# Kernel tuning notes

Hardware: AMD Instinct MI355X
Metric: run time of the kernel (lower is better)

## Reference

```python
import jax, jax.numpy as jnp
import numpy as np

CONF_THRESH = 0.01
TOP_K = 200
NMS_THRESH = 0.45


def decode(loc, dbox):
    # loc, dbox: [N,4]; dbox is (cx, cy, w, h)
    cxcy = dbox[:, :2] + loc[:, :2] * 0.1 * dbox[:, 2:]
    wh = dbox[:, 2:] * jnp.exp(loc[:, 2:] * 0.2)
    xymin = cxcy - wh * 0.5
    xymax = xymin + wh
    return jnp.concatenate([xymin, xymax], axis=1)  # [N,4] (x1,y1,x2,y2)


def nms_class(scores, boxes):
    # scores: [N], boxes: [N,4]. Mirrors torch greedy NMS with fixed-size padding.
    masked = jnp.where(scores > CONF_THRESH, scores, -1.0)
    topv, topi = jax.lax.top_k(masked, TOP_K)  # descending score, like idx[-top_k:] reversed
    cb = boxes[topi]  # [K,4]
    valid = topv > CONF_THRESH
    x1, y1, x2, y2 = cb[:, 0], cb[:, 1], cb[:, 2], cb[:, 3]
    area = (x2 - x1) * (y2 - y1)
    ar = jnp.arange(TOP_K)

    def body(i, keep):
        cur = keep[i]
        w = jnp.clip(jnp.minimum(x2, x2[i]) - jnp.maximum(x1, x1[i]), 0.0)
        h = jnp.clip(jnp.minimum(y2, y2[i]) - jnp.maximum(y1, y1[i]), 0.0)
        inter = w * h
        iou = inter / (area - inter + area[i])  # union = rem_area - inter + area[i]
        sup = (iou > NMS_THRESH) & (ar > i) & cur
        return keep & (~sup)

    keep = jax.lax.fori_loop(0, TOP_K, body, valid)
    # compact kept rows to the front, preserving descending-score order (stable sort)
    order = jnp.argsort(jnp.logical_not(keep), stable=True)
    count = jnp.sum(keep)
    rows = jnp.concatenate([topv[:, None], cb], axis=1)[order]  # [K,5] = (score, x1,y1,x2,y2)
    return jnp.where(ar[:, None] < count, rows, 0.0)


def setup_inputs() -> dict:
    key = jax.random.key(0)
    k1, k2, k3, k4 = jax.random.split(key, 4)
    B, N, C = 128, 8732, 21
    loc_data = jax.random.normal(k1, (B, N, 4), dtype=jnp.float32) * 0.5
    conf_data = jax.random.normal(k2, (B, N, C), dtype=jnp.float32)
    centers = jax.random.uniform(k3, (N, 2), dtype=jnp.float32)
    wh = jax.random.uniform(k4, (N, 2), dtype=jnp.float32, minval=0.02, maxval=0.3)
    dbox_list = jnp.concatenate([centers, wh], axis=1)
    return {"loc_data": loc_data, "conf_data": conf_data, "dbox_list": dbox_list}


def reference(loc_data, conf_data, dbox_list):
    conf = jax.nn.softmax(conf_data, axis=-1)                              # [B,N,C]
    boxes = jax.vmap(decode, in_axes=(0, None))(loc_data, dbox_list)       # [B,N,4]
    # vmap over classes (axis 1 of per-image conf) then over batch
    per_cls = jax.vmap(jax.vmap(nms_class, in_axes=(1, None)),
                       in_axes=(0, 0))(conf, boxes)                        # [B,C,K,5]
    return per_cls.at[:, 0].set(0.0)  # class 0 (background) is skipped in torch
```

## Files before the change

kernel.cpp:

```cpp
#include <hip/hip_runtime.h>

#define N_ANCH 8732
#define NCLS   21
#define BATCH  128
#define TOPK   200
#define CONF_T 0.01f
#define NMS_T  0.45f
#define HSIZE  1024
#define CAND_MAX 1024
#define NQ4    2183

__device__ __forceinline__ float exp_np(float x) {
    const float fx = floorf(__fmaf_rn(x, 1.442695040888963f, 0.5f));
    float t = __fmaf_rn(fx, -0.693359375f, x);
    t = __fmaf_rn(fx, 2.12194440e-4f, t);
    const float z = __fmul_rn(t, t);
    float y = 1.9875691500e-4f;
    y = __fmaf_rn(y, t, 1.3981999507e-3f);
    y = __fmaf_rn(y, t, 8.3334519073e-3f);
    y = __fmaf_rn(y, t, 4.1665795894e-2f);
    y = __fmaf_rn(y, t, 1.6666665459e-1f);
    y = __fmaf_rn(y, t, 5.0000001201e-1f);
    y = __fmaf_rn(y, z, t);
    y = __fadd_rn(y, 1.0f);
    return ldexpf(y, (int)fx);
}

__global__ __launch_bounds__(256) void prep_kernel(
    const float* __restrict__ loc, const float* __restrict__ conf,
    const float* __restrict__ dbox, float* __restrict__ probs,
    float* __restrict__ boxes)
{
    __shared__ float srow[256 * NCLS];
    const int block_row0 = blockIdx.x * 256;
    const float* cbase = conf + (size_t)block_row0 * NCLS;
    for (int i = threadIdx.x; i < 256 * NCLS; i += 256) srow[i] = cbase[i];
    __syncthreads();

    const int row = block_row0 + threadIdx.x;
    const int b = row / N_ANCH;
    const int n = row - b * N_ANCH;

    float e[NCLS];
    float m = srow[threadIdx.x * NCLS];
#pragma unroll
    for (int c = 1; c < NCLS; ++c) m = fmaxf(m, srow[threadIdx.x * NCLS + c]);
#pragma unroll
    for (int c = 0; c < NCLS; ++c)
        e[c] = exp_np(__fsub_rn(srow[threadIdx.x * NCLS + c], m));

    float acc[16];
#pragma unroll
    for (int j = 0; j < 16; ++j) acc[j] = e[j];
#pragma unroll
    for (int j = 0; j < 5; ++j) acc[j] = __fadd_rn(acc[j], e[16 + j]);
    float u[8];
#pragma unroll
    for (int j = 0; j < 8; ++j) u[j] = __fadd_rn(acc[j], acc[j + 8]);
    const float v0 = __fadd_rn(u[0], u[4]), v1 = __fadd_rn(u[1], u[5]);
    const float v2 = __fadd_rn(u[2], u[6]), v3 = __fadd_rn(u[3], u[7]);
    const float w0 = __fadd_rn(v0, v2), w1 = __fadd_rn(v1, v3);
    const float s  = __fadd_rn(w0, w1);

#pragma unroll
    for (int c = 1; c < NCLS; ++c)
        probs[((size_t)b * 20 + (c - 1)) * N_ANCH + n] = __fdiv_rn(e[c], s);

    const float4 l = *(const float4*)(loc + (size_t)row * 4);
    const float4 d = *(const float4*)(dbox + (size_t)n * 4);
    const float cx = __fmaf_rn(__fmul_rn(l.x, 0.1f), d.z, d.x);
    const float cy = __fmaf_rn(__fmul_rn(l.y, 0.1f), d.w, d.y);
    const float w  = __fmul_rn(d.z, exp_np(__fmul_rn(l.z, 0.2f)));
    const float h  = __fmul_rn(d.w, exp_np(__fmul_rn(l.w, 0.2f)));
    const float x1 = __fmaf_rn(w, -0.5f, cx);
    const float y1 = __fmaf_rn(h, -0.5f, cy);
    float4 o; o.x = x1; o.y = y1; o.z = __fadd_rn(x1, w); o.w = __fadd_rn(y1, h);
    *(float4*)(boxes + (size_t)row * 4) = o;
}

__global__ __launch_bounds__(256) void sel_kernel(
    const float* __restrict__ probs, const float* __restrict__ boxes,
    float* __restrict__ probs_mut)
{
    const int task = blockIdx.x;
    const int b = task / NCLS;
    const int c = task - b * NCLS;
    const int tid = threadIdx.x;
    if (c == 0) return;

    const float* prow = probs + ((size_t)b * 20 + (c - 1)) * N_ANCH;

    __shared__ int hist2[HSIZE * 2];
    __shared__ int wsum[4];
    __shared__ unsigned long long cand[CAND_MAX];
    __shared__ int selB;
    __shared__ int cnts[2];
    __shared__ unsigned ck[TOPK];
    __shared__ int  cn[TOPK];
    __shared__ unsigned sk[TOPK];
    __shared__ int  sn_[TOPK];

    const int wid = tid >> 6, lane = tid & 63;
    const int par = wid & 1;

    for (int i = tid; i < HSIZE * 2; i += 256) hist2[i] = 0;
    __syncthreads();
    for (int idx = tid; idx < NQ4; idx += 256) {
        const float4 v = *(const float4*)(prow + idx * 4);
        if (v.x > CONF_T) atomicAdd(&hist2[(int)((__float_as_uint(v.x) >> 16) - 0x3C23u) * 2 + par], 1);
        if (v.y > CONF_T) atomicAdd(&hist2[(int)((__float_as_uint(v.y) >> 16) - 0x3C23u) * 2 + par], 1);
        if (v.z > CONF_T) atomicAdd(&hist2[(int)((__float_as_uint(v.z) >> 16) - 0x3C23u) * 2 + par], 1);
        if (v.w > CONF_T) atomicAdd(&hist2[(int)((__float_as_uint(v.w) >> 16) - 0x3C23u) * 2 + par], 1);
    }
    __syncthreads();

    const int hbase = HSIZE - 4 * (tid + 1);
    int hb[4];
#pragma unroll
    for (int j = 0; j < 4; ++j) hb[j] = hist2[(hbase + j) * 2] + hist2[(hbase + j) * 2 + 1];
    const int part = hb[0] + hb[1] + hb[2] + hb[3];

    int incl = part;
#pragma unroll
    for (int off = 1; off < 64; off <<= 1) {
        const int v = __shfl_up(incl, off);
        if (lane >= off) incl += v;
    }
    if (lane == 63) wsum[wid] = incl;
    __syncthreads();
    int pre = 0;
    for (int w = 0; w < wid; ++w) pre += wsum[w];
    const int excl  = pre + incl - part;
    const int total = wsum[0] + wsum[1] + wsum[2] + wsum[3];
    if (tid == 0 && total < TOPK) selB = -1;
    if (excl < TOPK && excl + part >= TOPK) {
        int cacc = excl;
        for (int j = 3; j >= 0; --j) {
            if (cacc + hb[j] >= TOPK) { selB = hbase + j; break; }
            cacc += hb[j];
        }
    }
    if (tid == 0) { cnts[0] = 0; cnts[1] = 0; }
    __syncthreads();
    const int B = selB;

    for (int idx = tid; idx < NQ4; idx += 256) {
        const float4 v = *(const float4*)(prow + idx * 4);
        const float vv[4] = {v.x, v.y, v.z, v.w};
#pragma unroll
        for (int q = 0; q < 4; ++q) {
            const float s = vv[q];
            if (s > CONF_T) {
                const unsigned kk = __float_as_uint(s);
                const int bkt = (int)((kk >> 16) - 0x3C23u);
                if (bkt > B) {
                    const int p = atomicAdd(&cnts[0], 1);
                    ck[p] = kk; cn[p] = idx * 4 + q;
                } else if (bkt == B) {
                    const int qq = atomicAdd(&cnts[1], 1);
                    if (qq < CAND_MAX)
                        cand[qq] = ((unsigned long long)kk << 32) | (unsigned)(~(idx * 4 + q));
                }
            }
        }
    }
    __syncthreads();
    const int ndef  = cnts[0];
    const int slots = TOPK - ndef;
    int cc = cnts[1]; if (cc > CAND_MAX) cc = CAND_MAX;
    for (int i = tid; i < cc; i += 256) {
        const unsigned long long mine = cand[i];
        int rank = 0;
        for (int j = 0; j < cc; ++j) rank += (cand[j] > mine) ? 1 : 0;
        if (rank < slots) {
            const int p = atomicAdd(&cnts[0], 1);
            ck[p] = (unsigned)(mine >> 32);
            cn[p] = (int)(~(unsigned)mine);
        }
    }
    __syncthreads();
    const int cnt_arr = cnts[0];

    if (tid < TOPK) { sk[tid] = 0u; sn_[tid] = -1; }
    __syncthreads();
    if (tid < cnt_arr) {
        const unsigned mk = ck[tid];
        const int mn = cn[tid];
        int rank = 0;
        for (int j = 0; j < cnt_arr; ++j) {
            const unsigned kj = ck[j];
            rank += (kj > mk || (kj == mk && cn[j] < mn)) ? 1 : 0;
        }
        sk[rank] = mk; sn_[rank] = mn;
    }
    __syncthreads();

    float* selrow = probs_mut + ((size_t)b * 20 + (c - 1)) * N_ANCH;
    for (int i = tid; i < TOPK; i += 256) {
        const int n = sn_[i];
        float scv = 0.f;
        float4 bx = make_float4(0.f, 0.f, 0.f, 0.f);
        if (n >= 0) {
            scv = __uint_as_float(sk[i]);
            bx = *(const float4*)(boxes + ((size_t)b * N_ANCH + n) * 4);
        }
        float* dst = selrow + i * 5;
        dst[0] = scv; dst[1] = bx.x; dst[2] = bx.y; dst[3] = bx.z; dst[4] = bx.w;
    }
}

__global__ __launch_bounds__(256) void nms_kernel(
    const float* __restrict__ sel, float* __restrict__ out)
{
    const int wv = threadIdx.x >> 6;
    const int lane = threadIdx.x & 63;
    const int task = blockIdx.x * 4 + wv;
    const int b = task / NCLS;
    const int c = task - b * NCLS;
    float* obase = out + (size_t)task * (TOPK * 5);
    __shared__ float outrow[4][TOPK * 5];

    if (c == 0) {
        for (int i = lane; i < TOPK * 5; i += 64) obase[i] = 0.f;
        return;
    }
    const float* srow = sel + ((size_t)b * 20 + (c - 1)) * N_ANCH;

    float sc[4], x1[4], y1[4], x2[4], y2[4], ar[4];
    int kp[4];
#pragma unroll
    for (int s = 0; s < 4; ++s) {
        const int i = s * 64 + lane;
        float a = 0.f, p1 = 0.f, p2 = 0.f, p3 = 0.f, p4 = 0.f;
        if (i < TOPK) {
            a  = srow[i * 5 + 0];
            p1 = srow[i * 5 + 1]; p2 = srow[i * 5 + 2];
            p3 = srow[i * 5 + 3]; p4 = srow[i * 5 + 4];
        }
        sc[s] = a; x1[s] = p1; y1[s] = p2; x2[s] = p3; y2[s] = p4;
        ar[s] = __fmul_rn(__fsub_rn(p3, p1), __fsub_rn(p4, p2));
        kp[s] = (a > CONF_T) ? 1 : 0;
    }

#pragma unroll
    for (int si = 0; si < 4; ++si) {
        const int ilim = (si < 3) ? 64 : (TOPK - 192);
        for (int o = 0; o < ilim; ++o) {
            const int ki = __shfl(kp[si], o);
            if (!ki) continue;
            const float ix1 = __shfl(x1[si], o);
            const float iy1 = __shfl(y1[si], o);
            const float ix2 = __shfl(x2[si], o);
            const float iy2 = __shfl(y2[si], o);
            const float ia  = __shfl(ar[si], o);
            if (lane > o && (si * 64 + lane) < TOPK && kp[si]) {
                const float w = fmaxf(0.f, __fsub_rn(fminf(x2[si], ix2), fmaxf(x1[si], ix1)));
                const float h = fmaxf(0.f, __fsub_rn(fminf(y2[si], iy2), fmaxf(y1[si], iy1)));
                const float inter = __fmul_rn(w, h);
                const float denom = __fadd_rn(__fsub_rn(ar[si], inter), ia);
                if (__fdiv_rn(inter, denom) > NMS_T) kp[si] = 0;
            }
#pragma unroll
            for (int s = si + 1; s < 4; ++s) {
                const int j = s * 64 + lane;
                if (j < TOPK && kp[s]) {
                    const float w = fmaxf(0.f, __fsub_rn(fminf(x2[s], ix2), fmaxf(x1[s], ix1)));
                    const float h = fmaxf(0.f, __fsub_rn(fminf(y2[s], iy2), fmaxf(y1[s], iy1)));
                    const float inter = __fmul_rn(w, h);
                    const float denom = __fadd_rn(__fsub_rn(ar[s], inter), ia);
                    if (__fdiv_rn(inter, denom) > NMS_T) kp[s] = 0;
                }
            }
        }
    }

    unsigned long long msk[4];
#pragma unroll
    for (int s = 0; s < 4; ++s) msk[s] = __ballot(kp[s] != 0);
    const unsigned long long lt = (1ull << lane) - 1ull;

    for (int i = lane; i < TOPK * 5; i += 64) outrow[wv][i] = 0.f;
    int base = 0;
#pragma unroll
    for (int s = 0; s < 4; ++s) {
        if (kp[s]) {
            const int d = base + (int)__popcll(msk[s] & lt);
            outrow[wv][d * 5 + 0] = sc[s];
            outrow[wv][d * 5 + 1] = x1[s];
            outrow[wv][d * 5 + 2] = y1[s];
            outrow[wv][d * 5 + 3] = x2[s];
            outrow[wv][d * 5 + 4] = y2[s];
        }
        base += (int)__popcll(msk[s]);
    }
    for (int i = lane; i < TOPK * 5; i += 64) obase[i] = outrow[wv][i];
}

extern "C" void kernel_launch(void* const* d_in, const int* in_sizes, int n_in,
                              void* d_out, int out_size, void* d_ws, size_t ws_size,
                              hipStream_t stream) {
    (void)in_sizes; (void)n_in; (void)out_size; (void)ws_size;
    const float* loc  = (const float*)d_in[0];
    const float* conf = (const float*)d_in[1];
    const float* dbox = (const float*)d_in[2];
    float* out   = (float*)d_out;
    float* probs = (float*)d_ws;
    float* boxes = (float*)((char*)d_ws + (size_t)BATCH * 20 * N_ANCH * 4);

    prep_kernel<<<(BATCH * N_ANCH) / 256, 256, 0, stream>>>(loc, conf, dbox, probs, boxes);
    sel_kernel<<<BATCH * NCLS, 256, 0, stream>>>(probs, boxes, probs);
    nms_kernel<<<(BATCH * NCLS) / 4, 256, 0, stream>>>(probs, out);
}
```

Before: 198.3 us.

## Restructure NMS into parallel IoU bitmask build plus serial mask sweep

Each (batch,class) task now gets a full 256-thread block instead of one wavefront. The four waves compute a full pairwise IoU suppression bitmask matrix in parallel into shared memory. A cheap serial sweep over 64-bit masks then resolves greedy keep, and compaction uses popcount/bit selection. This removes the serialized shuffle-and-divide chain per kept box. The cost is computing all pairwise IoUs regardless of early suppression, a redundant per-thread sweep, and four times more blocks.

Result: slower. 277.7 us (+40.1%).

```diff
diff --git a/kernel.cpp b/kernel.cpp
--- a/kernel.cpp
+++ b/kernel.cpp
@@ -212,88 +212,113 @@
 __global__ __launch_bounds__(256) void nms_kernel(
     const float* __restrict__ sel, float* __restrict__ out)
 {
-    const int wv = threadIdx.x >> 6;
-    const int lane = threadIdx.x & 63;
-    const int task = blockIdx.x * 4 + wv;
+    const int task = blockIdx.x;
     const int b = task / NCLS;
     const int c = task - b * NCLS;
     float* obase = out + (size_t)task * (TOPK * 5);
-    __shared__ float outrow[4][TOPK * 5];
+    const int tid = threadIdx.x;
+    const int wv = tid >> 6, lane = tid & 63;
 
     if (c == 0) {
-        for (int i = lane; i < TOPK * 5; i += 64) obase[i] = 0.f;
+        for (int i = tid; i < TOPK * 5; i += 256) obase[i] = 0.f;
         return;
     }
     const float* srow = sel + ((size_t)b * 20 + (c - 1)) * N_ANCH;
 
-    float sc[4], x1[4], y1[4], x2[4], y2[4], ar[4];
-    int kp[4];
+    __shared__ float bxs[TOPK * 5];
+    __shared__ unsigned long long rows[TOPK][4];
+    __shared__ unsigned long long Ksh[4];
+
+    for (int i = tid; i < TOPK * 5; i += 256) bxs[i] = srow[i];
+    __syncthreads();
+
+    float jx1[4], jy1[4], jx2[4], jy2[4], jar[4];
+    int jval[4];
 #pragma unroll
     for (int s = 0; s < 4; ++s) {
-        const int i = s * 64 + lane;
+        const int j = s * 64 + lane;
         float a = 0.f, p1 = 0.f, p2 = 0.f, p3 = 0.f, p4 = 0.f;
-        if (i < TOPK) {
-            a  = srow[i * 5 + 0];
-            p1 = srow[i * 5 + 1]; p2 = srow[i * 5 + 2];
-            p3 = srow[i * 5 + 3]; p4 = srow[i * 5 + 4];
-        }
-        sc[s] = a; x1[s] = p1; y1[s] = p2; x2[s] = p3; y2[s] = p4;
-        ar[s] = __fmul_rn(__fsub_rn(p3, p1), __fsub_rn(p4, p2));
-        kp[s] = (a > CONF_T) ? 1 : 0;
-    }
-
-#pragma unroll
-    for (int si = 0; si < 4; ++si) {
-        const int ilim = (si < 3) ? 64 : (TOPK - 192);
-        for (int o = 0; o < ilim; ++o) {
-            const int ki = __shfl(kp[si], o);
-            if (!ki) continue;
-            const float ix1 = __shfl(x1[si], o);
-            const float iy1 = __shfl(y1[si], o);
-            const float ix2 = __shfl(x2[si], o);
-            const float iy2 = __shfl(y2[si], o);
-            const float ia  = __shfl(ar[si], o);
-            if (lane > o && (si * 64 + lane) < TOPK && kp[si]) {
-                const float w = fmaxf(0.f, __fsub_rn(fminf(x2[si], ix2), fmaxf(x1[si], ix1)));
-                const float h = fmaxf(0.f, __fsub_rn(fminf(y2[si], iy2), fmaxf(y1[si], iy1)));
-                const float inter = __fmul_rn(w, h);
-                const float denom = __fadd_rn(__fsub_rn(ar[si], inter), ia);
-                if (__fdiv_rn(inter, denom) > NMS_T) kp[si] = 0;
-            }
-#pragma unroll
-            for (int s = si + 1; s < 4; ++s) {
-                const int j = s * 64 + lane;
-                if (j < TOPK && kp[s]) {
-                    const float w = fmaxf(0.f, __fsub_rn(fminf(x2[s], ix2), fmaxf(x1[s], ix1)));
-                    const float h = fmaxf(0.f, __fsub_rn(fminf(y2[s], iy2), fmaxf(y1[s], iy1)));
-                    const float inter = __fmul_rn(w, h);
-                    const float denom = __fadd_rn(__fsub_rn(ar[s], inter), ia);
-                    if (__fdiv_rn(inter, denom) > NMS_T) kp[s] = 0;
-                }
-            }
-        }
-    }
-
-    unsigned long long msk[4];
-#pragma unroll
-    for (int s = 0; s < 4; ++s) msk[s] = __ballot(kp[s] != 0);
-    const unsigned long long lt = (1ull << lane) - 1ull;
-
-    for (int i = lane; i < TOPK * 5; i += 64) outrow[wv][i] = 0.f;
-    int base = 0;
-#pragma unroll
-    for (int s = 0; s < 4; ++s) {
-        if (kp[s]) {
-            const int d = base + (int)__popcll(msk[s] & lt);
-            outrow[wv][d * 5 + 0] = sc[s];
-            outrow[wv][d * 5 + 1] = x1[s];
-            outrow[wv][d * 5 + 2] = y1[s];
-            outrow[wv][d * 5 + 3] = x2[s];
-            outrow[wv][d * 5 + 4] = y2[s];
-        }
-        base += (int)__popcll(msk[s]);
-    }
-    for (int i = lane; i < TOPK * 5; i += 64) obase[i] = outrow[wv][i];
+        if (j < TOPK) {
+            a = bxs[j * 5 + 0];
+            p1 = bxs[j * 5 + 1]; p2 = bxs[j * 5 + 2];
+            p3 = bxs[j * 5 + 3]; p4 = bxs[j * 5 + 4];
+        }
+        jx1[s] = p1; jy1[s] = p2; jx2[s] = p3; jy2[s] = p4;
+        jar[s] = __fmul_rn(__fsub_rn(p3, p1), __fsub_rn(p4, p2));
+        jval[s] = (a > CONF_T) ? 1 : 0;
+    }
+    if (wv == 0) {
+#pragma unroll
+        for (int s = 0; s < 4; ++s) {
+            const unsigned long long m = __ballot(jval[s] != 0);
+            if (lane == 0) Ksh[s] = m;
+        }
+    }
+
+    const int i0 = wv * 50;
+    for (int i = i0; i < i0 + 50; ++i) {
+        const float ix1 = bxs[i * 5 + 1], iy1 = bxs[i * 5 + 2];
+        const float ix2 = bxs[i * 5 + 3], iy2 = bxs[i * 5 + 4];
+        const float ia  = __fmul_rn(__fsub_rn(ix2, ix1), __fsub_rn(iy2, iy1));
+#pragma unroll
+        for (int s = 0; s < 4; ++s) {
+            const int j = s * 64 + lane;
+            const float w = fmaxf(0.f, __fsub_rn(fminf(jx2[s], ix2), fmaxf(jx1[s], ix1)));
+            const float h = fmaxf(0.f, __fsub_rn(fminf(jy2[s], iy2), fmaxf(jy1[s], iy1)));
+            const float inter = __fmul_rn(w, h);
+            const float denom = __fadd_rn(__fsub_rn(jar[s], inter), ia);
+            const float iou = __fdiv_rn(inter, denom);
+            const bool bit = (j < TOPK) && (j > i) && (iou > NMS_T);
+            const unsigned long long m = __ballot(bit);
+            if (lane == 0) rows[i][s] = m;
+        }
+    }
+    __syncthreads();
+
+    unsigned long long K0 = Ksh[0], K1 = Ksh[1], K2 = Ksh[2], K3 = Ksh[3];
+#pragma unroll
+    for (int w4 = 0; w4 < 4; ++w4) {
+        const int lim = (w4 < 3) ? 64 : (TOPK - 192);
+        for (int o = 0; o < lim; ++o) {
+            const int i = w4 * 64 + o;
+            unsigned long long live;
+            if (w4 == 0) live = (K0 >> o) & 1ull;
+            else if (w4 == 1) live = (K1 >> o) & 1ull;
+            else if (w4 == 2) live = (K2 >> o) & 1ull;
+            else live = (K3 >> o) & 1ull;
+            const unsigned long long msel = 0ull - live;
+            K0 &= ~(rows[i][0] & msel);
+            K1 &= ~(rows[i][1] & msel);
+            K2 &= ~(rows[i][2] & msel);
+            K3 &= ~(rows[i][3] & msel);
+        }
+    }
+
+    if (tid < TOPK) {
+        const int d = tid;
+        const int c0 = (int)__popcll(K0), c1 = (int)__popcll(K1),
+                  c2 = (int)__popcll(K2), c3 = (int)__popcll(K3);
+        const int totalk = c0 + c1 + c2 + c3;
+        float o0 = 0.f, o1 = 0.f, o2 = 0.f, o3 = 0.f, o4 = 0.f;
+        if (d < totalk) {
+            int r = d;
+            unsigned long long x;
+            int wbase;
+            if (r < c0)               { x = K0; wbase = 0;   }
+            else if (r < c0 + c1)     { x = K1; wbase = 64;  r -= c0; }
+            else if (r < c0 + c1 + c2){ x = K2; wbase = 128; r -= c0 + c1; }
+            else                      { x = K3; wbase = 192; r -= c0 + c1 + c2; }
+            for (int t = 0; t < r; ++t) x &= x - 1ull;
+            const int p = wbase + (__ffsll((unsigned long long)x) - 1);
+            o0 = bxs[p * 5 + 0]; o1 = bxs[p * 5 + 1]; o2 = bxs[p * 5 + 2];
+            o3 = bxs[p * 5 + 3]; o4 = bxs[p * 5 + 4];
+        }
+        obase[d * 5 + 0] = o0;
+        obase[d * 5 + 1] = o1;
+        obase[d * 5 + 2] = o2;
+        obase[d * 5 + 3] = o3;
+        obase[d * 5 + 4] = o4;
+    }
 }
 
 extern "C" void kernel_launch(void* const* d_in, const int* in_sizes, int n_in,
@@ -309,5 +334,5 @@
 
     prep_kernel<<<(BATCH * N_ANCH) / 256, 256, 0, stream>>>(loc, conf, dbox, probs, boxes);
     sel_kernel<<<BATCH * NCLS, 256, 0, stream>>>(probs, boxes, probs);
-    nms_kernel<<<(BATCH * NCLS) / 4, 256, 0, stream>>>(probs, out);
-}
+    nms_kernel<<<BATCH * NCLS, 256, 0, stream>>>(probs, out);
+}
```
